# Performance work log

Hardware: AMD Instinct MI355X
Metric: run time of the kernel (lower is better)

## Reference

```python
import jax, jax.numpy as jnp
from jax import lax
import numpy as np

BLUR = 1e-4      # sinkhorn_blur
P_NORM = 2       # sinkhorn_p
SCALING = 0.9
NUM_SG = 8
LOCAL_W = 1.0
GLOBAL_W = 0.5
BATCH = 4096
DIM = 256


def _cost(X, Y):
    # geomloss cost for p=2: ||x-y||^2 / 2, computed via GEMM (no [P,m,m,d] broadcast)
    x2 = jnp.sum(X * X, axis=-1)                      # [P,m]
    y2 = jnp.sum(Y * Y, axis=-1)                      # [P,m]
    xy = jnp.einsum('pid,pjd->pij', X, Y)             # [P,m,m]
    sq = jnp.clip(x2[:, :, None] + y2[:, None, :] - 2.0 * xy, 0.0)
    return 0.5 * sq


def _softmin(eps, C, h):
    # softmin_eps(C, h)_i = -eps * logsumexp_j (h_j - C_ij / eps)
    return -eps * jax.nn.logsumexp(h[:, None, :] - C / eps, axis=-1)


def _eps_schedule():
    # epsilon-scaling: from (diameter bound)^p down to blur^p by factor scaling^p
    eps0 = 4.0 * DIM                 # static upper bound on sq. diameter of N(0,1) features
    target = BLUR ** P_NORM
    ratio = SCALING ** P_NORM
    n = int(np.ceil(np.log(target / eps0) / np.log(ratio)))
    return np.maximum(eps0 * ratio ** np.arange(n + 1), target).astype(np.float32)


def _sinkhorn_pairs(X, Y):
    # Debiased Sinkhorn divergence for a batch of pairs; X,Y: [P,m,d] -> [P]
    P, m, d = X.shape
    loga = -jnp.log(float(m))  # uniform weights
    Cxy = _cost(X, Y)
    Cyx = jnp.swapaxes(Cxy, 1, 2)
    Cxx = _cost(X, X)
    Cyy = _cost(Y, Y)
    # geomloss runs the scaling iterations detached, then one last extrapolation with grad
    Cs = tuple(lax.stop_gradient(C) for C in (Cxy, Cyx, Cxx, Cyy))
    eps_list = jnp.asarray(_eps_schedule())

    def body(carry, eps):
        f, g, px, py = carry
        ft = _softmin(eps, Cs[0], loga + g / eps)
        gt = _softmin(eps, Cs[1], loga + f / eps)
        pxt = _softmin(eps, Cs[2], loga + px / eps)
        pyt = _softmin(eps, Cs[3], loga + py / eps)
        return (0.5 * (f + ft), 0.5 * (g + gt), 0.5 * (px + pxt), 0.5 * (py + pyt)), None

    init = tuple(jnp.zeros((P, m), X.dtype) for _ in range(4))
    (f, g, px, py), _ = lax.scan(body, init, eps_list)

    eps_f = eps_list[-1]
    f_fin = _softmin(eps_f, Cxy, loga + lax.stop_gradient(g) / eps_f)
    g_fin = _softmin(eps_f, Cyx, loga + lax.stop_gradient(f) / eps_f)
    px_fin = _softmin(eps_f, Cxx, loga + lax.stop_gradient(px) / eps_f)
    py_fin = _softmin(eps_f, Cyy, loga + lax.stop_gradient(py) / eps_f)
    # S_eps(x,y) = <a, f - p_x> + <b, g - p_y>, uniform weights -> means
    return jnp.mean(f_fin - px_fin, axis=-1) + jnp.mean(g_fin - py_fin, axis=-1)


def _forward(features, labels, subgroups):
    B, d = features.shape
    m_local = B // (2 * NUM_SG)   # samples per (class, subgroup) cell
    m_global = B // NUM_SG        # samples per subgroup
    pi, pj = np.triu_indices(NUM_SG, k=1)  # 28 subgroup pairs

    # local: per-class subgroup cells (balanced inputs -> static sizes)
    cells = []
    for lbl in range(2):
        for sg in range(NUM_SG):
            idx = jnp.nonzero((labels == lbl) & (subgroups == sg), size=m_local)[0]
            cells.append(features[idx])
    cells = jnp.stack(cells).reshape(2, NUM_SG, m_local, d)
    X = cells[:, pi].reshape(-1, m_local, d)   # [56,m,d]
    Y = cells[:, pj].reshape(-1, m_local, d)
    # (sum_real/28 + sum_fake/28)/2 == mean over all 56 pairs
    local_loss = jnp.mean(_sinkhorn_pairs(X, Y))

    gcells = jnp.stack([features[jnp.nonzero(subgroups == sg, size=m_global)[0]]
                        for sg in range(NUM_SG)])  # [8,m_g,d]
    global_loss = jnp.mean(_sinkhorn_pairs(gcells[pi], gcells[pj]))

    return LOCAL_W * local_loss + GLOBAL_W * global_loss


def setup_inputs():
    key = jax.random.key(0)
    features = jax.random.normal(key, (BATCH, DIM), dtype=jnp.float32)
    ar = jnp.arange(BATCH, dtype=jnp.int32)
    labels = ar % 2                      # balanced real/fake
    subgroups = (ar // 2) % NUM_SG       # balanced subgroups per class
    return {"features": features, "labels": labels, "subgroups": subgroups}


def reference(features, labels, subgroups):
    return _forward(features, labels, subgroups)
```

## Files before the change

### kernel.cpp

```cpp
#include <hip/hip_runtime.h>
#include <math.h>

#define LOG2E 1.4426950408889634f
#define LN2   0.6931471805599453f

typedef short    short8  __attribute__((ext_vector_type(8)));
typedef float    floatx4 __attribute__((ext_vector_type(4)));
typedef _Float16 half8   __attribute__((ext_vector_type(8)));

__constant__ int c_pi[28] = {0,0,0,0,0,0,0,1,1,1,1,1,1,2,2,2,2,2,3,3,3,3,4,4,4,5,5,6};
__constant__ int c_pj[28] = {1,2,3,4,5,6,7,2,3,4,5,6,7,3,4,5,6,7,4,5,6,7,5,6,7,6,7,7};

__device__ unsigned short g_cellsL[16*256*256];
__device__ unsigned short g_cellsG[8*512*256];
__device__ float g_x2L[16*256];
__device__ float g_x2G[8*512];
__device__ int   g_idxL[16*256];
__device__ int   g_idxG[8*512];
__device__ _Float16 g_CL[128*256*256];
__device__ _Float16 g_CG[64*512*512];
__device__ float g_fL[2][56*256];
__device__ float g_gL[2][56*256];
__device__ float g_pxL[2][16*256];
__device__ float g_fG[2][28*512];
__device__ float g_gG[2][28*512];
__device__ float g_pxG[2][8*512];

__device__ __forceinline__ unsigned short f2bf(float f) {
    unsigned u = __float_as_uint(f);
    u += 0x7fffu + ((u >> 16) & 1u);
    return (unsigned short)(u >> 16);
}

__global__ void k_index(const int* __restrict__ labels, const int* __restrict__ subg) {
    int b = blockIdx.x, lane = threadIdx.x;
    int want_l, want_s, cap; int* out;
    if (b < 16) { want_l = b >> 3; want_s = b & 7; cap = 256; out = g_idxL + b*256; }
    else        { want_l = -1;     want_s = b - 16; cap = 512; out = g_idxG + (b-16)*512; }
    int cnt = 0;
    for (int base = 0; base < 4096; base += 64) {
        int i = base + lane;
        bool m = (subg[i] == want_s) && (want_l < 0 || labels[i] == want_l);
        unsigned long long mask = __ballot(m);
        int pos = cnt + __popcll(mask & ((1ull << lane) - 1ull));
        if (m && pos < cap) out[pos] = i;
        cnt += __popcll(mask);
    }
}

__global__ void k_gather(const float* __restrict__ feat) {
    int wv = blockIdx.x*4 + (threadIdx.x >> 6);
    int lane = threadIdx.x & 63;
    const float* src; unsigned short* dst; float* x2out;
    if (wv < 4096) {
        int c = wv >> 8, row = wv & 255;
        src = feat + (size_t)g_idxL[c*256+row]*256;
        dst = g_cellsL + (size_t)(c*256+row)*256;
        x2out = g_x2L + c*256 + row;
    } else {
        int v = wv - 4096; int c = v >> 9, row = v & 511;
        src = feat + (size_t)g_idxG[c*512+row]*256;
        dst = g_cellsG + (size_t)(c*512+row)*256;
        x2out = g_x2G + c*512 + row;
    }
    floatx4 v4 = *(const floatx4*)(src + lane*4);
    float s = v4[0]*v4[0] + v4[1]*v4[1] + v4[2]*v4[2] + v4[3]*v4[3];
    unsigned lo = (unsigned)f2bf(v4[0]) | ((unsigned)f2bf(v4[1]) << 16);
    unsigned hi = (unsigned)f2bf(v4[2]) | ((unsigned)f2bf(v4[3]) << 16);
    unsigned* d32 = (unsigned*)dst;
    d32[lane*2] = lo; d32[lane*2+1] = hi;
    for (int o = 32; o; o >>= 1) s += __shfl_xor(s, o);
    if (lane == 0) *x2out = s;
}

__global__ void k_gemm() {
    int job = blockIdx.x*4 + (threadIdx.x >> 6);
    int lane = threadIdx.x & 63;
    const unsigned short *A, *B; _Float16* Cout; const float *x2a, *x2b;
    int m, ti, tj;
    if (job < 32768) {
        int mm = job >> 8, t = job & 255; ti = t >> 4; tj = t & 15; m = 256;
        int ca, cb;
        if (mm < 56)       { int lbl = mm/28,  q = mm%28;  ca = lbl*8 + c_pi[q]; cb = lbl*8 + c_pj[q]; }
        else if (mm < 112) { int p = mm-56; int lbl = p/28, q = p%28;
                             ca = lbl*8 + c_pj[q]; cb = lbl*8 + c_pi[q]; }
        else               { int c = mm-112; ca = cb = c; }
        A = g_cellsL + (size_t)ca*65536; B = g_cellsL + (size_t)cb*65536;
        x2a = g_x2L + ca*256; x2b = g_x2L + cb*256;
        Cout = g_CL + (size_t)mm*65536;
    } else {
        int jj = job - 32768; int mm = jj >> 10, t = jj & 1023; ti = t >> 5; tj = t & 31; m = 512;
        int ca, cb;
        if (mm < 28)      { ca = c_pi[mm];    cb = c_pj[mm]; }
        else if (mm < 56) { ca = c_pj[mm-28]; cb = c_pi[mm-28]; }
        else              { ca = cb = mm-56; }
        A = g_cellsG + (size_t)ca*131072; B = g_cellsG + (size_t)cb*131072;
        x2a = g_x2G + ca*512; x2b = g_x2G + cb*512;
        Cout = g_CG + (size_t)mm*262144;
    }
    int r = lane & 15, quad = lane >> 4;
    const unsigned short* Ap = A + (size_t)(ti*16 + r)*256 + quad*8;
    const unsigned short* Bp = B + (size_t)(tj*16 + r)*256 + quad*8;
    floatx4 acc = {0.f, 0.f, 0.f, 0.f};
    #pragma unroll
    for (int k = 0; k < 256; k += 32) {
        short8 av = *(const short8*)(Ap + k);
        short8 bv = *(const short8*)(Bp + k);
        acc = __builtin_amdgcn_mfma_f32_16x16x32_bf16(av, bv, acc, 0, 0, 0);
    }
    int jc = tj*16 + r;
    float y2 = x2b[jc];
    #pragma unroll
    for (int rr = 0; rr < 4; rr++) {
        int ir = ti*16 + quad*4 + rr;
        float v = x2a[ir] + y2 - 2.f*acc[rr];
        Cout[(size_t)ir*m + jc] = (_Float16)(0.5f*fmaxf(v, 0.f));
    }
}

__global__ void k_init() {
    int t = blockIdx.x*256 + threadIdx.x;
    if      (t < 14336) g_fL[0][t] = 0.f;
    else if (t < 28672) g_gL[0][t-14336] = 0.f;
    else if (t < 32768) g_pxL[0][t-28672] = 0.f;
    else if (t < 47104) g_fG[0][t-32768] = 0.f;
    else if (t < 61440) g_gG[0][t-47104] = 0.f;
    else                g_pxG[0][t-61440] = 0.f;
}

template<int M>
__device__ __forceinline__ void sm_pass(const _Float16* __restrict__ C,
    const float* __restrict__ hsrc, const float* __restrict__ fold,
    float* __restrict__ fout, int r0, float eps, float inv_eps, float loga,
    int hard, int fin)
{
    const int W = (M == 256) ? 16 : 32;
    int tid = threadIdx.x, lane = tid & 63, w = tid >> 6;
    int co = (M == 256) ? (lane & 31) : lane;
    float h[8];
    floatx4 h0 = *(const floatx4*)(hsrc + co*8);
    floatx4 h1 = *(const floatx4*)(hsrc + co*8 + 4);
    #pragma unroll
    for (int k = 0; k < 4; k++) { h[k] = loga + h0[k]*inv_eps; h[4+k] = loga + h1[k]*inv_eps; }
    int rbase = (M == 256) ? (r0 + w*16) : (r0 + w*8);
    int rowst = (M == 256) ? 2 : 1;
    int radd  = (M == 256) ? (lane >> 5) : 0;
    bool wr   = (M == 256) ? ((lane & 31) == 0) : (lane == 0);

    const _Float16* cp = C + (size_t)(rbase + radd)*M + co*8;
    half8 cv = *(const half8*)cp;
    #pragma unroll
    for (int s = 0; s < 8; s++) {
        half8 cvn;
        if (s < 7) cvn = *(const half8*)(cp + (size_t)rowst*M);
        float tv[8]; float mx = -3.4e38f;
        #pragma unroll
        for (int k = 0; k < 8; k++) {
            float t = h[k] - (float)cv[k]*inv_eps;
            tv[k] = t; mx = fmaxf(mx, t);
        }
        #pragma unroll
        for (int o = W; o; o >>= 1) mx = fmaxf(mx, __shfl_xor(mx, o));
        float ft;
        if (!hard) {
            float sum = 0.f;
            #pragma unroll
            for (int k = 0; k < 8; k++) sum += exp2f((tv[k] - mx)*LOG2E);
            #pragma unroll
            for (int o = W; o; o >>= 1) sum += __shfl_xor(sum, o);
            ft = -eps*(mx + LN2*__log2f(sum));
        } else {
            ft = -eps*mx;
        }
        if (wr) {
            int row = rbase + rowst*s + radd;
            fout[row] = fin ? ft : 0.5f*(fold[row] + ft);
        }
        cv = cvn; cp += (size_t)rowst*M;
    }
}

__global__ void k_iter(float eps, float inv_eps, int par, int hard, int fin) {
    const float LGA = -5.545177444479562f;
    const float LGG = -6.238324625039508f;
    int b = blockIdx.x;
    int po = par, pn = par ^ 1;
    if (b < 512) {
        int m = b >> 2, r0 = (b & 3)*64;
        const _Float16* C = g_CL + (size_t)m*65536;
        const float *h, *fo; float* fn;
        if (m < 56)       { h = g_gL[po]+m*256;  fo = g_fL[po]+m*256;  fn = g_fL[pn]+m*256; }
        else if (m < 112) { int p = m-56;  h = g_fL[po]+p*256;  fo = g_gL[po]+p*256;  fn = g_gL[pn]+p*256; }
        else              { int c = m-112; h = g_pxL[po]+c*256; fo = h;               fn = g_pxL[pn]+c*256; }
        sm_pass<256>(C, h, fo, fn, r0, eps, inv_eps, LGA, hard, fin);
    } else {
        int v = b - 512; int m = v >> 4, r0 = (v & 15)*32;
        const _Float16* C = g_CG + (size_t)m*262144;
        const float *h, *fo; float* fn;
        if (m < 28)      { h = g_gG[po]+m*512;  fo = g_fG[po]+m*512;  fn = g_fG[pn]+m*512; }
        else if (m < 56) { int p = m-28;  h = g_fG[po]+p*512;  fo = g_gG[po]+p*512;  fn = g_gG[pn]+p*512; }
        else             { int c = m-56;  h = g_pxG[po]+c*512; fo = h;               fn = g_pxG[pn]+c*512; }
        sm_pass<512>(C, h, fo, fn, r0, eps, inv_eps, LGG, hard, fin);
    }
}

__global__ void k_combine(float* __restrict__ out) {
    __shared__ float red[4][4];
    int tid = threadIdx.x;
    float sfg_l = 0.f, spx_l = 0.f, sfg_g = 0.f, spx_g = 0.f;
    for (int i = tid; i < 14336; i += 256) sfg_l += g_fL[1][i] + g_gL[1][i];
    for (int i = tid; i < 4096;  i += 256) spx_l += g_pxL[1][i];
    for (int i = tid; i < 14336; i += 256) sfg_g += g_fG[1][i] + g_gG[1][i];
    for (int i = tid; i < 4096;  i += 256) spx_g += g_pxG[1][i];
    for (int o = 32; o; o >>= 1) {
        sfg_l += __shfl_xor(sfg_l, o); spx_l += __shfl_xor(spx_l, o);
        sfg_g += __shfl_xor(sfg_g, o); spx_g += __shfl_xor(spx_g, o);
    }
    int w = tid >> 6;
    if ((tid & 63) == 0) { red[0][w] = sfg_l; red[1][w] = spx_l; red[2][w] = sfg_g; red[3][w] = spx_g; }
    __syncthreads();
    if (tid == 0) {
        float SL = red[0][0]+red[0][1]+red[0][2]+red[0][3];
        float PL = red[1][0]+red[1][1]+red[1][2]+red[1][3];
        float SG = red[2][0]+red[2][1]+red[2][2]+red[2][3];
        float PG = red[3][0]+red[3][1]+red[3][2]+red[3][3];
        float local_l  = SL/14336.f - PL/2048.f;
        float global_l = SG/14336.f - PG/2048.f;
        out[0] = 1.0f*local_l + 0.5f*global_l;
    }
}

extern "C" void kernel_launch(void* const* d_in, const int* in_sizes, int n_in,
                              void* d_out, int out_size, void* d_ws, size_t ws_size,
                              hipStream_t stream) {
    (void)in_sizes; (void)n_in; (void)out_size; (void)d_ws; (void)ws_size;
    const float* feat  = (const float*)d_in[0];
    const int* labels  = (const int*)d_in[1];
    const int* subg    = (const int*)d_in[2];

    k_index <<<24,    64, 0, stream>>>(labels, subg);
    k_gather<<<2048, 256, 0, stream>>>(feat);
    k_gemm  <<<24576,256, 0, stream>>>();
    k_init  <<<256,  256, 0, stream>>>();

    double eps0 = 4.0*256.0, ratio = 0.9*0.9, target = 1e-4*1e-4;
    int n = (int)ceil(log(target/eps0)/log(ratio));
    float ef = 1e-8f;
    for (int k = 0; k <= n; k++) {
        double e = eps0 * pow(ratio, (double)k);
        if (e < target) e = target;
        ef = (float)e;
        int hard = (ef < 1e-5f) ? 1 : 0;
        k_iter<<<1536, 256, 0, stream>>>(ef, (float)(1.0/(double)ef), k & 1, hard, 0);
    }
    k_iter<<<1536, 256, 0, stream>>>(ef, (float)(1.0/(double)ef), 0, 1, 1);
    k_combine<<<1, 256, 0, stream>>>((float*)d_out);
}
```

Baseline: 2.015 ms.

## Drop transposed cost matrices and compute g-update via column-wise online logsumexp

Stops materialising the transposed Cyx cost matrices in the GEMM and instead computes the g potential update with a new column-reduction routine that reads Cxy directly. It uses a streaming max/sum logsumexp over rows, then a cross-lane and shared-memory merge. Block indexing is also remapped with an XCD-style interleave (b&7) so blocks sharing a matrix land together. This cuts GEMM work and cost-matrix storage and reads by about 44%. In exchange it adds more exp2 calls per element in the online rescaling and a __syncthreads in the column blocks.

```diff
diff --git a/kernel.cpp b/kernel.cpp
--- a/kernel.cpp
+++ b/kernel.cpp
@@ -17,8 +17,8 @@
 __device__ float g_x2G[8*512];
 __device__ int   g_idxL[16*256];
 __device__ int   g_idxG[8*512];
-__device__ _Float16 g_CL[128*256*256];
-__device__ _Float16 g_CG[64*512*512];
+__device__ _Float16 g_CL[72*256*256];
+__device__ _Float16 g_CG[36*512*512];
 __device__ float g_fL[2][56*256];
 __device__ float g_gL[2][56*256];
 __device__ float g_pxL[2][16*256];
@@ -78,22 +78,19 @@
     int lane = threadIdx.x & 63;
     const unsigned short *A, *B; _Float16* Cout; const float *x2a, *x2b;
     int m, ti, tj;
-    if (job < 32768) {
+    if (job < 18432) {
         int mm = job >> 8, t = job & 255; ti = t >> 4; tj = t & 15; m = 256;
         int ca, cb;
-        if (mm < 56)       { int lbl = mm/28,  q = mm%28;  ca = lbl*8 + c_pi[q]; cb = lbl*8 + c_pj[q]; }
-        else if (mm < 112) { int p = mm-56; int lbl = p/28, q = p%28;
-                             ca = lbl*8 + c_pj[q]; cb = lbl*8 + c_pi[q]; }
-        else               { int c = mm-112; ca = cb = c; }
+        if (mm < 56) { int lbl = mm/28, q = mm%28; ca = lbl*8 + c_pi[q]; cb = lbl*8 + c_pj[q]; }
+        else         { int c = mm-56; ca = cb = c; }
         A = g_cellsL + (size_t)ca*65536; B = g_cellsL + (size_t)cb*65536;
         x2a = g_x2L + ca*256; x2b = g_x2L + cb*256;
         Cout = g_CL + (size_t)mm*65536;
     } else {
-        int jj = job - 32768; int mm = jj >> 10, t = jj & 1023; ti = t >> 5; tj = t & 31; m = 512;
+        int jj = job - 18432; int mm = jj >> 10, t = jj & 1023; ti = t >> 5; tj = t & 31; m = 512;
         int ca, cb;
-        if (mm < 28)      { ca = c_pi[mm];    cb = c_pj[mm]; }
-        else if (mm < 56) { ca = c_pj[mm-28]; cb = c_pi[mm-28]; }
-        else              { ca = cb = mm-56; }
+        if (mm < 28) { ca = c_pi[mm]; cb = c_pj[mm]; }
+        else         { ca = cb = mm-28; }
         A = g_cellsG + (size_t)ca*131072; B = g_cellsG + (size_t)cb*131072;
         x2a = g_x2G + ca*512; x2b = g_x2G + cb*512;
         Cout = g_CG + (size_t)mm*262144;
@@ -151,7 +148,7 @@
     half8 cv = *(const half8*)cp;
     #pragma unroll
     for (int s = 0; s < 8; s++) {
-        half8 cvn;
+        half8 cvn = cv;
         if (s < 7) cvn = *(const half8*)(cp + (size_t)rowst*M);
         float tv[8]; float mx = -3.4e38f;
         #pragma unroll
@@ -180,27 +177,118 @@
     }
 }
 
+template<int M>
+__device__ __forceinline__ void sm_col(const _Float16* __restrict__ C,
+    const float* __restrict__ frow, const float* __restrict__ gold,
+    float* __restrict__ gout, int c0, float eps, float inv_eps, float loga,
+    int hard, int fin)
+{
+    int tid = threadIdx.x, lane = tid & 63, w = tid >> 6;
+    const float i2  = inv_eps * LOG2E;
+    const float lg2 = loga * LOG2E;
+    int colg = lane & 7;
+    int rsub = (lane >> 3) + w*8;
+    const int STEPS = M/32;
+    float m2[8], ss[8];
+    #pragma unroll
+    for (int k = 0; k < 8; k++) { m2[k] = -3.4e38f; ss[k] = 0.f; }
+    const _Float16* cp = C + (size_t)rsub*M + c0 + colg*8;
+    half8 cv = *(const half8*)cp;
+    float fr = frow[rsub];
+    #pragma unroll
+    for (int s2 = 0; s2 < STEPS; s2++) {
+        half8 cvn = cv; float frn = fr;
+        if (s2 < STEPS-1) { cvn = *(const half8*)(cp + (size_t)32*M); frn = frow[rsub + 32*(s2+1)]; }
+        float a2 = lg2 + fr * i2;
+        if (!hard) {
+            #pragma unroll
+            for (int k = 0; k < 8; k++) {
+                float u  = a2 - (float)cv[k]*i2;
+                float mn = fmaxf(m2[k], u);
+                ss[k] = ss[k]*exp2f(m2[k]-mn) + exp2f(u-mn);
+                m2[k] = mn;
+            }
+        } else {
+            #pragma unroll
+            for (int k = 0; k < 8; k++) {
+                float u = a2 - (float)cv[k]*i2;
+                m2[k] = fmaxf(m2[k], u);
+            }
+        }
+        cv = cvn; fr = frn; cp += (size_t)32*M;
+    }
+    #pragma unroll
+    for (int o = 8; o < 64; o <<= 1) {
+        #pragma unroll
+        for (int k = 0; k < 8; k++) {
+            float mo = __shfl_xor(m2[k], o);
+            float so = __shfl_xor(ss[k], o);
+            float mn = fmaxf(m2[k], mo);
+            if (!hard) ss[k] = ss[k]*exp2f(m2[k]-mn) + so*exp2f(mo-mn);
+            m2[k] = mn;
+        }
+    }
+    __shared__ float smm[4][64], sms[4][64];
+    if (lane < 8) {
+        #pragma unroll
+        for (int k = 0; k < 8; k++) { smm[w][lane*8+k] = m2[k]; sms[w][lane*8+k] = ss[k]; }
+    }
+    __syncthreads();
+    if (tid < 64) {
+        float m = smm[0][tid], s = sms[0][tid];
+        #pragma unroll
+        for (int ww = 1; ww < 4; ww++) {
+            float mo = smm[ww][tid], so = sms[ww][tid];
+            float mn = fmaxf(m, mo);
+            if (!hard) s = s*exp2f(m-mn) + so*exp2f(mo-mn);
+            m = mn;
+        }
+        float gt = hard ? (-eps*LN2*m) : (-eps*LN2*(m + __log2f(s)));
+        int c = c0 + tid;
+        gout[c] = fin ? gt : 0.5f*(gold[c] + gt);
+    }
+}
+
 __global__ void k_iter(float eps, float inv_eps, int par, int hard, int fin) {
     const float LGA = -5.545177444479562f;
     const float LGG = -6.238324625039508f;
     int b = blockIdx.x;
+    int x = b & 7, s = b >> 3;
     int po = par, pn = par ^ 1;
-    if (b < 512) {
-        int m = b >> 2, r0 = (b & 3)*64;
-        const _Float16* C = g_CL + (size_t)m*65536;
-        const float *h, *fo; float* fn;
-        if (m < 56)       { h = g_gL[po]+m*256;  fo = g_fL[po]+m*256;  fn = g_fL[pn]+m*256; }
-        else if (m < 112) { int p = m-56;  h = g_fL[po]+p*256;  fo = g_gL[po]+p*256;  fn = g_gL[pn]+p*256; }
-        else              { int c = m-112; h = g_pxL[po]+c*256; fo = h;               fn = g_pxL[pn]+c*256; }
-        sm_pass<256>(C, h, fo, fn, r0, eps, inv_eps, LGA, hard, fin);
+    if (s < 56) {
+        int q = s >> 3, j = s & 7, p = q*8 + x;
+        const _Float16* C = g_CL + (size_t)p*65536;
+        if (j < 4)
+            sm_pass<256>(C, g_gL[po]+p*256, g_fL[po]+p*256, g_fL[pn]+p*256,
+                         j*64, eps, inv_eps, LGA, hard, fin);
+        else
+            sm_col<256>(C, g_fL[po]+p*256, g_gL[po]+p*256, g_gL[pn]+p*256,
+                        (j-4)*64, eps, inv_eps, LGA, hard, fin);
+    } else if (s < 64) {
+        int t = s - 56; int c = (t >> 2)*8 + x;
+        const _Float16* C = g_CL + (size_t)(56+c)*65536;
+        const float* h = g_pxL[po]+c*256;
+        sm_pass<256>(C, h, h, g_pxL[pn]+c*256, (t&3)*64, eps, inv_eps, LGA, hard, fin);
     } else {
-        int v = b - 512; int m = v >> 4, r0 = (v & 15)*32;
-        const _Float16* C = g_CG + (size_t)m*262144;
-        const float *h, *fo; float* fn;
-        if (m < 28)      { h = g_gG[po]+m*512;  fo = g_fG[po]+m*512;  fn = g_fG[pn]+m*512; }
-        else if (m < 56) { int p = m-28;  h = g_fG[po]+p*512;  fo = g_gG[po]+p*512;  fn = g_gG[pn]+p*512; }
-        else             { int c = m-56;  h = g_pxG[po]+c*512; fo = h;               fn = g_pxG[pn]+c*512; }
-        sm_pass<512>(C, h, fo, fn, r0, eps, inv_eps, LGG, hard, fin);
+        int gp = (x < 4) ? 4 : 3;
+        int t = s - 64;
+        if (t < 24*gp) {
+            int q = t/24, j = t%24, p = q*8 + x;
+            const _Float16* C = g_CG + (size_t)p*262144;
+            if (j < 16)
+                sm_pass<512>(C, g_gG[po]+p*512, g_fG[po]+p*512, g_fG[pn]+p*512,
+                             j*32, eps, inv_eps, LGG, hard, fin);
+            else
+                sm_col<512>(C, g_fG[po]+p*512, g_gG[po]+p*512, g_gG[pn]+p*512,
+                            (j-16)*64, eps, inv_eps, LGG, hard, fin);
+        } else {
+            t -= 24*gp;
+            if (t < 16) {
+                const _Float16* C = g_CG + (size_t)(28+x)*262144;
+                const float* h = g_pxG[po]+x*512;
+                sm_pass<512>(C, h, h, g_pxG[pn]+x*512, t*32, eps, inv_eps, LGG, hard, fin);
+            }
+        }
     }
 }
 
@@ -240,7 +328,7 @@
 
     k_index <<<24,    64, 0, stream>>>(labels, subg);
     k_gather<<<2048, 256, 0, stream>>>(feat);
-    k_gemm  <<<24576,256, 0, stream>>>();
+    k_gemm  <<<13824,256, 0, stream>>>();
     k_init  <<<256,  256, 0, stream>>>();
 
     double eps0 = 4.0*256.0, ratio = 0.9*0.9, target = 1e-4*1e-4;
@@ -251,8 +339,8 @@
         if (e < target) e = target;
         ef = (float)e;
         int hard = (ef < 1e-5f) ? 1 : 0;
-        k_iter<<<1536, 256, 0, stream>>>(ef, (float)(1.0/(double)ef), k & 1, hard, 0);
-    }
-    k_iter<<<1536, 256, 0, stream>>>(ef, (float)(1.0/(double)ef), 0, 1, 1);
+        k_iter<<<1408, 256, 0, stream>>>(ef, (float)(1.0/(double)ef), k & 1, hard, 0);
+    }
+    k_iter<<<1408, 256, 0, stream>>>(ef, (float)(1.0/(double)ef), 0, 1, 1);
     k_combine<<<1, 256, 0, stream>>>((float*)d_out);
 }
```

New measurement: 2.229 ms. 1.11x slower.

## Fuse all Sinkhorn iterations into one persistent LDS-resident kernel with group barriers

Applied to the files above, without the earlier changes.

Replaces the roughly 123 per-epsilon k_iter launches with a single persistent kernel of 216 blocks. Each block keeps its slice of the cost matrix in LDS and loops over all epsilon rounds on chip. The transposed cost matrices are dropped: g is computed as a column-wise online logsumexp over the same C tile. Global-pair blocks that split one matrix four ways exchange partial (max, sum) pairs through global memory behind spin-wait group barriers. This removes per-launch overhead and the repeated HBM reads of C and halves GEMM work, but it relies on all 216 blocks being co-resident (one per CU) for the barriers to avoid deadlock, and the barrier has a guard that breaks out silently.

```diff
diff --git a/kernel.cpp b/kernel.cpp
--- a/kernel.cpp
+++ b/kernel.cpp
@@ -17,19 +17,29 @@
 __device__ float g_x2G[8*512];
 __device__ int   g_idxL[16*256];
 __device__ int   g_idxG[8*512];
-__device__ _Float16 g_CL[128*256*256];
-__device__ _Float16 g_CG[64*512*512];
-__device__ float g_fL[2][56*256];
-__device__ float g_gL[2][56*256];
-__device__ float g_pxL[2][16*256];
-__device__ float g_fG[2][28*512];
-__device__ float g_gG[2][28*512];
-__device__ float g_pxG[2][8*512];
+__device__ _Float16 g_CL[72*256*256];
+__device__ _Float16 g_CG[36*512*512];
+__device__ unsigned long long g_xch[28][4][512];
+__device__ float g_xpx[8][4][128];
+__device__ unsigned g_bar[36];
+__device__ float g_acc[4];
 
 __device__ __forceinline__ unsigned short f2bf(float f) {
     unsigned u = __float_as_uint(f);
     u += 0x7fffu + ((u >> 16) & 1u);
     return (unsigned short)(u >> 16);
+}
+__device__ __forceinline__ void xst64(unsigned long long* p, unsigned long long v) {
+    __hip_atomic_store(p, v, __ATOMIC_RELAXED, __HIP_MEMORY_SCOPE_AGENT);
+}
+__device__ __forceinline__ unsigned long long xld64(const unsigned long long* p) {
+    return __hip_atomic_load(p, __ATOMIC_RELAXED, __HIP_MEMORY_SCOPE_AGENT);
+}
+__device__ __forceinline__ void xstf(float* p, float v) {
+    __hip_atomic_store(p, v, __ATOMIC_RELAXED, __HIP_MEMORY_SCOPE_AGENT);
+}
+__device__ __forceinline__ float xldf(const float* p) {
+    return __hip_atomic_load(p, __ATOMIC_RELAXED, __HIP_MEMORY_SCOPE_AGENT);
 }
 
 __global__ void k_index(const int* __restrict__ labels, const int* __restrict__ subg) {
@@ -78,22 +88,19 @@
     int lane = threadIdx.x & 63;
     const unsigned short *A, *B; _Float16* Cout; const float *x2a, *x2b;
     int m, ti, tj;
-    if (job < 32768) {
+    if (job < 18432) {
         int mm = job >> 8, t = job & 255; ti = t >> 4; tj = t & 15; m = 256;
         int ca, cb;
-        if (mm < 56)       { int lbl = mm/28,  q = mm%28;  ca = lbl*8 + c_pi[q]; cb = lbl*8 + c_pj[q]; }
-        else if (mm < 112) { int p = mm-56; int lbl = p/28, q = p%28;
-                             ca = lbl*8 + c_pj[q]; cb = lbl*8 + c_pi[q]; }
-        else               { int c = mm-112; ca = cb = c; }
+        if (mm < 56) { int lbl = mm/28, q = mm%28; ca = lbl*8 + c_pi[q]; cb = lbl*8 + c_pj[q]; }
+        else         { int c = mm-56; ca = cb = c; }
         A = g_cellsL + (size_t)ca*65536; B = g_cellsL + (size_t)cb*65536;
         x2a = g_x2L + ca*256; x2b = g_x2L + cb*256;
         Cout = g_CL + (size_t)mm*65536;
     } else {
-        int jj = job - 32768; int mm = jj >> 10, t = jj & 1023; ti = t >> 5; tj = t & 31; m = 512;
+        int jj = job - 18432; int mm = jj >> 10, t = jj & 1023; ti = t >> 5; tj = t & 31; m = 512;
         int ca, cb;
-        if (mm < 28)      { ca = c_pi[mm];    cb = c_pj[mm]; }
-        else if (mm < 56) { ca = c_pj[mm-28]; cb = c_pi[mm-28]; }
-        else              { ca = cb = mm-56; }
+        if (mm < 28) { ca = c_pi[mm]; cb = c_pj[mm]; }
+        else         { ca = cb = mm-28; }
         A = g_cellsG + (size_t)ca*131072; B = g_cellsG + (size_t)cb*131072;
         x2a = g_x2G + ca*512; x2b = g_x2G + cb*512;
         Cout = g_CG + (size_t)mm*262144;
@@ -119,114 +126,366 @@
 }
 
 __global__ void k_init() {
-    int t = blockIdx.x*256 + threadIdx.x;
-    if      (t < 14336) g_fL[0][t] = 0.f;
-    else if (t < 28672) g_gL[0][t-14336] = 0.f;
-    else if (t < 32768) g_pxL[0][t-28672] = 0.f;
-    else if (t < 47104) g_fG[0][t-32768] = 0.f;
-    else if (t < 61440) g_gG[0][t-47104] = 0.f;
-    else                g_pxG[0][t-61440] = 0.f;
-}
-
-template<int M>
-__device__ __forceinline__ void sm_pass(const _Float16* __restrict__ C,
-    const float* __restrict__ hsrc, const float* __restrict__ fold,
-    float* __restrict__ fout, int r0, float eps, float inv_eps, float loga,
-    int hard, int fin)
-{
-    const int W = (M == 256) ? 16 : 32;
-    int tid = threadIdx.x, lane = tid & 63, w = tid >> 6;
-    int co = (M == 256) ? (lane & 31) : lane;
-    float h[8];
-    floatx4 h0 = *(const floatx4*)(hsrc + co*8);
-    floatx4 h1 = *(const floatx4*)(hsrc + co*8 + 4);
+    int t = threadIdx.x;
+    if (t < 36) g_bar[t] = 0u;
+    if (t < 4)  g_acc[t] = 0.f;
+}
+
+__device__ __forceinline__ void group_bar(int gid, unsigned tgt) {
+    if (threadIdx.x == 0) {
+        __hip_atomic_fetch_add(&g_bar[gid], 1u, __ATOMIC_RELEASE, __HIP_MEMORY_SCOPE_AGENT);
+        int guard = 0;
+        while (__hip_atomic_load(&g_bar[gid], __ATOMIC_ACQUIRE, __HIP_MEMORY_SCOPE_AGENT) < tgt) {
+            __builtin_amdgcn_s_sleep(2);
+            if (++guard > 5000000) break;
+        }
+    }
+    __syncthreads();
+}
+
+extern __shared__ char smem[];
+__global__ void __launch_bounds__(512) k_solve() {
+    _Float16* sC = (_Float16*)smem;
+    float* scr  = (float*)(smem + 131072);
+    float* sg   = (float*)(smem + 147456);
+    float* sf   = (float*)(smem + 151552);
+    float* sred = (float*)(smem + 155648);
+    int b = blockIdx.x, tid = threadIdx.x, lane = tid & 63, w = tid >> 6;
+
+    int role, gid = -1, q = 0;
+    const _Float16* Csrc; float loga;
+    if (b < 112)      { role = 2; gid = b >> 2; q = b & 3;
+                        Csrc = g_CG + (size_t)gid*262144 + (size_t)q*65536;
+                        loga = -6.238324625039508f; }
+    else if (b < 144) { role = 3; int t = b - 112; int c = t >> 2; q = t & 3; gid = 28 + c;
+                        Csrc = g_CG + (size_t)(28+c)*262144 + (size_t)q*65536;
+                        loga = -6.238324625039508f; }
+    else if (b < 200) { role = 0; int p = b - 144;
+                        Csrc = g_CL + (size_t)p*65536;
+                        loga = -5.545177444479562f; }
+    else              { role = 1; int c = b - 200;
+                        Csrc = g_CL + (size_t)(56+c)*65536;
+                        loga = -5.545177444479562f; }
+
+    for (int i = tid; i < 8192; i += 512)
+        ((floatx4*)sC)[i] = ((const floatx4*)Csrc)[i];
+    for (int i = tid; i < 1024; i += 512) { sg[i] = 0.f; sf[i] = 0.f; }
+    __syncthreads();
+
+    const double ratio = 0.9*0.9;
+    int po = 0;
+    for (int round = 0; round < 123; round++) {
+        int fin = (round == 122);
+        double e = 1024.0 * pow(ratio, (double)(fin ? 121 : round));
+        if (e < 1e-8) e = 1e-8;
+        float ef = (float)e;
+        float inv = (float)(1.0/e);
+        int hard = (ef < 1e-5f) ? 1 : 0;
+        float i2  = inv * LOG2E;
+        float lg2 = loga * LOG2E;
+        float meps = -ef * LN2;
+        int pn = po ^ 1;
+
+        if (role == 2) {
+            const float* gp = sg + po*512;
+            const float* fpo = sf + po*512;
+            float* fpn = sf + pn*512;
+            float h2[8];
+            #pragma unroll
+            for (int k = 0; k < 8; k++) h2[k] = lg2 + gp[lane*8+k]*i2;
+            float m2[8], ssv[8];
+            #pragma unroll
+            for (int k = 0; k < 8; k++) { m2[k] = -3.4e38f; ssv[k] = 0.f; }
+            #pragma unroll 4
+            for (int s = 0; s < 16; s++) {
+                int row = w*16 + s;
+                half8 cv = *(const half8*)(sC + row*512 + lane*8);
+                float fr = fpo[row];
+                float a2 = lg2 + fr*i2;
+                float tv[8]; float mx = -3.4e38f;
+                #pragma unroll
+                for (int k = 0; k < 8; k++) {
+                    float d = (float)cv[k]*(-i2);
+                    float t = h2[k] + d; tv[k] = t; mx = fmaxf(mx, t);
+                    float u = a2 + d;
+                    float mn = fmaxf(m2[k], u);
+                    if (!hard) ssv[k] = ssv[k]*exp2f(m2[k]-mn) + exp2f(u-mn);
+                    m2[k] = mn;
+                }
+                #pragma unroll
+                for (int o = 32; o; o >>= 1) mx = fmaxf(mx, __shfl_xor(mx, o));
+                float ft;
+                if (!hard) {
+                    float sum = 0.f;
+                    #pragma unroll
+                    for (int k = 0; k < 8; k++) sum += exp2f(tv[k]-mx);
+                    #pragma unroll
+                    for (int o = 32; o; o >>= 1) sum += __shfl_xor(sum, o);
+                    ft = meps*(mx + __log2f(sum));
+                } else ft = meps*mx;
+                if (lane == 0) fpn[row] = fin ? ft : 0.5f*(fr + ft);
+            }
+            if (w >= 4) {
+                float* pm = scr + (w-4)*512; float* ps = scr + 2048 + (w-4)*512;
+                #pragma unroll
+                for (int k = 0; k < 8; k++) { pm[lane*8+k] = m2[k]; ps[lane*8+k] = ssv[k]; }
+            }
+            __syncthreads();
+            if (w < 4) {
+                const float* pm = scr + w*512; const float* ps = scr + 2048 + w*512;
+                #pragma unroll
+                for (int k = 0; k < 8; k++) {
+                    float mo = pm[lane*8+k], so = ps[lane*8+k];
+                    float mn = fmaxf(m2[k], mo);
+                    if (!hard) ssv[k] = ssv[k]*exp2f(m2[k]-mn) + so*exp2f(mo-mn);
+                    m2[k] = mn;
+                }
+            }
+            __syncthreads();
+            if (w >= 1 && w < 4) {
+                float* pm = scr + (w-1)*512; float* ps = scr + 2048 + (w-1)*512;
+                #pragma unroll
+                for (int k = 0; k < 8; k++) { pm[lane*8+k] = m2[k]; ps[lane*8+k] = ssv[k]; }
+            }
+            __syncthreads();
+            if (w == 0) {
+                #pragma unroll
+                for (int j = 0; j < 3; j++) {
+                    const float* pm = scr + j*512; const float* ps = scr + 2048 + j*512;
+                    #pragma unroll
+                    for (int k = 0; k < 8; k++) {
+                        float mo = pm[lane*8+k], so = ps[lane*8+k];
+                        float mn = fmaxf(m2[k], mo);
+                        if (!hard) ssv[k] = ssv[k]*exp2f(m2[k]-mn) + so*exp2f(mo-mn);
+                        m2[k] = mn;
+                    }
+                }
+                #pragma unroll
+                for (int k = 0; k < 8; k++)
+                    xst64(&g_xch[gid][q][lane*8+k],
+                          (unsigned long long)__float_as_uint(m2[k]) |
+                          ((unsigned long long)__float_as_uint(ssv[k]) << 32));
+            }
+            __syncthreads();
+            group_bar(gid, 4u*(unsigned)(round+1));
+            {
+                int c = tid;
+                unsigned long long v0 = xld64(&g_xch[gid][0][c]);
+                unsigned long long v1 = xld64(&g_xch[gid][1][c]);
+                unsigned long long v2 = xld64(&g_xch[gid][2][c]);
+                unsigned long long v3 = xld64(&g_xch[gid][3][c]);
+                float a0 = __uint_as_float((unsigned)v0), b0 = __uint_as_float((unsigned)(v0 >> 32));
+                float a1 = __uint_as_float((unsigned)v1), b1 = __uint_as_float((unsigned)(v1 >> 32));
+                float a2m = __uint_as_float((unsigned)v2), b2 = __uint_as_float((unsigned)(v2 >> 32));
+                float a3 = __uint_as_float((unsigned)v3), b3 = __uint_as_float((unsigned)(v3 >> 32));
+                float m = fmaxf(fmaxf(a0, a1), fmaxf(a2m, a3));
+                float gt;
+                if (!hard) {
+                    float s = b0*exp2f(a0-m) + b1*exp2f(a1-m) + b2*exp2f(a2m-m) + b3*exp2f(a3-m);
+                    gt = meps*(m + __log2f(s));
+                } else gt = meps*m;
+                sg[pn*512+c] = fin ? gt : 0.5f*(sg[po*512+c] + gt);
+            }
+            __syncthreads();
+        } else if (role == 3) {
+            const float* pp = sg + po*512;
+            float* ppn = sg + pn*512;
+            float h2[8];
+            #pragma unroll
+            for (int k = 0; k < 8; k++) h2[k] = lg2 + pp[lane*8+k]*i2;
+            #pragma unroll 4
+            for (int s = 0; s < 16; s++) {
+                int row = w*16 + s;
+                half8 cv = *(const half8*)(sC + row*512 + lane*8);
+                float tv[8]; float mx = -3.4e38f;
+                #pragma unroll
+                for (int k = 0; k < 8; k++) {
+                    float t = h2[k] - (float)cv[k]*i2;
+                    tv[k] = t; mx = fmaxf(mx, t);
+                }
+                #pragma unroll
+                for (int o = 32; o; o >>= 1) mx = fmaxf(mx, __shfl_xor(mx, o));
+                float ft;
+                if (!hard) {
+                    float sum = 0.f;
+                    #pragma unroll
+                    for (int k = 0; k < 8; k++) sum += exp2f(tv[k]-mx);
+                    #pragma unroll
+                    for (int o = 32; o; o >>= 1) sum += __shfl_xor(sum, o);
+                    ft = meps*(mx + __log2f(sum));
+                } else ft = meps*mx;
+                if (lane == 0) {
+                    float old = pp[q*128 + row];
+                    xstf(&g_xpx[gid-28][q][row], fin ? ft : 0.5f*(old + ft));
+                }
+            }
+            __syncthreads();
+            group_bar(gid, 4u*(unsigned)(round+1));
+            { int c = tid; ppn[c] = xldf(&g_xpx[gid-28][c>>7][c&127]); }
+            __syncthreads();
+        } else if (role == 0) {
+            const float* gp = sg + po*512;
+            const float* fpo = sf + po*512;
+            float* fpn = sf + pn*512;
+            int co = lane & 31, radd = lane >> 5;
+            float h2[8];
+            #pragma unroll
+            for (int k = 0; k < 8; k++) h2[k] = lg2 + gp[co*8+k]*i2;
+            float m2[8], ssv[8];
+            #pragma unroll
+            for (int k = 0; k < 8; k++) { m2[k] = -3.4e38f; ssv[k] = 0.f; }
+            #pragma unroll 4
+            for (int s = 0; s < 16; s++) {
+                int row = w*32 + 2*s + radd;
+                half8 cv = *(const half8*)(sC + row*256 + co*8);
+                float fr = fpo[row];
+                float a2 = lg2 + fr*i2;
+                float tv[8]; float mx = -3.4e38f;
+                #pragma unroll
+                for (int k = 0; k < 8; k++) {
+                    float d = (float)cv[k]*(-i2);
+                    float t = h2[k] + d; tv[k] = t; mx = fmaxf(mx, t);
+                    float u = a2 + d;
+                    float mn = fmaxf(m2[k], u);
+                    if (!hard) ssv[k] = ssv[k]*exp2f(m2[k]-mn) + exp2f(u-mn);
+                    m2[k] = mn;
+                }
+                #pragma unroll
+                for (int o = 16; o; o >>= 1) mx = fmaxf(mx, __shfl_xor(mx, o));
+                float ft;
+                if (!hard) {
+                    float sum = 0.f;
+                    #pragma unroll
+                    for (int k = 0; k < 8; k++) sum += exp2f(tv[k]-mx);
+                    #pragma unroll
+                    for (int o = 16; o; o >>= 1) sum += __shfl_xor(sum, o);
+                    ft = meps*(mx + __log2f(sum));
+                } else ft = meps*mx;
+                if ((lane & 31) == 0) fpn[row] = fin ? ft : 0.5f*(fr + ft);
+            }
+            #pragma unroll
+            for (int k = 0; k < 8; k++) {
+                float mo = __shfl_xor(m2[k], 32), so = __shfl_xor(ssv[k], 32);
+                float mn = fmaxf(m2[k], mo);
+                if (!hard) ssv[k] = ssv[k]*exp2f(m2[k]-mn) + so*exp2f(mo-mn);
+                m2[k] = mn;
+            }
+            if (w >= 4 && lane < 32) {
+                float* pm = scr + (w-4)*256; float* ps = scr + 1024 + (w-4)*256;
+                #pragma unroll
+                for (int k = 0; k < 8; k++) { pm[co*8+k] = m2[k]; ps[co*8+k] = ssv[k]; }
+            }
+            __syncthreads();
+            if (w < 4 && lane < 32) {
+                const float* pm = scr + w*256; const float* ps = scr + 1024 + w*256;
+                #pragma unroll
+                for (int k = 0; k < 8; k++) {
+                    float mo = pm[co*8+k], so = ps[co*8+k];
+                    float mn = fmaxf(m2[k], mo);
+                    if (!hard) ssv[k] = ssv[k]*exp2f(m2[k]-mn) + so*exp2f(mo-mn);
+                    m2[k] = mn;
+                }
+            }
+            __syncthreads();
+            if (w >= 1 && w < 4 && lane < 32) {
+                float* pm = scr + (w-1)*256; float* ps = scr + 1024 + (w-1)*256;
+                #pragma unroll
+                for (int k = 0; k < 8; k++) { pm[co*8+k] = m2[k]; ps[co*8+k] = ssv[k]; }
+            }
+            __syncthreads();
+            if (w == 0 && lane < 32) {
+                #pragma unroll
+                for (int j = 0; j < 3; j++) {
+                    const float* pm = scr + j*256; const float* ps = scr + 1024 + j*256;
+                    #pragma unroll
+                    for (int k = 0; k < 8; k++) {
+                        float mo = pm[co*8+k], so = ps[co*8+k];
+                        float mn = fmaxf(m2[k], mo);
+                        if (!hard) ssv[k] = ssv[k]*exp2f(m2[k]-mn) + so*exp2f(mo-mn);
+                        m2[k] = mn;
+                    }
+                }
+                #pragma unroll
+                for (int k = 0; k < 8; k++) {
+                    int c = co*8 + k;
+                    float gt = hard ? meps*m2[k] : meps*(m2[k] + __log2f(ssv[k]));
+                    sg[pn*512+c] = fin ? gt : 0.5f*(sg[po*512+c] + gt);
+                }
+            }
+            __syncthreads();
+        } else {
+            const float* pp = sg + po*512;
+            float* ppn = sg + pn*512;
+            int co = lane & 31, radd = lane >> 5;
+            float h2[8];
+            #pragma unroll
+            for (int k = 0; k < 8; k++) h2[k] = lg2 + pp[co*8+k]*i2;
+            #pragma unroll 4
+            for (int s = 0; s < 16; s++) {
+                int row = w*32 + 2*s + radd;
+                half8 cv = *(const half8*)(sC + row*256 + co*8);
+                float tv[8]; float mx = -3.4e38f;
+                #pragma unroll
+                for (int k = 0; k < 8; k++) {
+                    float t = h2[k] - (float)cv[k]*i2;
+                    tv[k] = t; mx = fmaxf(mx, t);
+                }
+                #pragma unroll
+                for (int o = 16; o; o >>= 1) mx = fmaxf(mx, __shfl_xor(mx, o));
+                float ft;
+                if (!hard) {
+                    float sum = 0.f;
+                    #pragma unroll
+                    for (int k = 0; k < 8; k++) sum += exp2f(tv[k]-mx);
+                    #pragma unroll
+                    for (int o = 16; o; o >>= 1) sum += __shfl_xor(sum, o);
+                    ft = meps*(mx + __log2f(sum));
+                } else ft = meps*mx;
+                if ((lane & 31) == 0) {
+                    float old = pp[row];
+                    ppn[row] = fin ? ft : 0.5f*(old + ft);
+                }
+            }
+            __syncthreads();
+        }
+        po = pn;
+    }
+
+    float v = 0.f, v2 = 0.f; int idx, idx2 = -1;
+    if (role == 0)      { if (tid < 256) v = sf[po*512+tid] + sg[po*512+tid]; idx = 0; }
+    else if (role == 1) { if (tid < 256) v = sg[po*512+tid]; idx = 1; }
+    else if (role == 2) { if (tid < 128) v = sf[po*512+tid]; idx = 2;
+                          if (q == 0) { v2 = sg[po*512+tid]; idx2 = 2; } }
+    else                { if (tid < 128) v = sg[po*512 + q*128 + tid]; idx = 3; }
     #pragma unroll
-    for (int k = 0; k < 4; k++) { h[k] = loga + h0[k]*inv_eps; h[4+k] = loga + h1[k]*inv_eps; }
-    int rbase = (M == 256) ? (r0 + w*16) : (r0 + w*8);
-    int rowst = (M == 256) ? 2 : 1;
-    int radd  = (M == 256) ? (lane >> 5) : 0;
-    bool wr   = (M == 256) ? ((lane & 31) == 0) : (lane == 0);
-
-    const _Float16* cp = C + (size_t)(rbase + radd)*M + co*8;
-    half8 cv = *(const half8*)cp;
-    #pragma unroll
-    for (int s = 0; s < 8; s++) {
-        half8 cvn;
-        if (s < 7) cvn = *(const half8*)(cp + (size_t)rowst*M);
-        float tv[8]; float mx = -3.4e38f;
-        #pragma unroll
-        for (int k = 0; k < 8; k++) {
-            float t = h[k] - (float)cv[k]*inv_eps;
-            tv[k] = t; mx = fmaxf(mx, t);
-        }
-        #pragma unroll
-        for (int o = W; o; o >>= 1) mx = fmaxf(mx, __shfl_xor(mx, o));
-        float ft;
-        if (!hard) {
-            float sum = 0.f;
-            #pragma unroll
-            for (int k = 0; k < 8; k++) sum += exp2f((tv[k] - mx)*LOG2E);
-            #pragma unroll
-            for (int o = W; o; o >>= 1) sum += __shfl_xor(sum, o);
-            ft = -eps*(mx + LN2*__log2f(sum));
-        } else {
-            ft = -eps*mx;
-        }
-        if (wr) {
-            int row = rbase + rowst*s + radd;
-            fout[row] = fin ? ft : 0.5f*(fold[row] + ft);
-        }
-        cv = cvn; cp += (size_t)rowst*M;
-    }
-}
-
-__global__ void k_iter(float eps, float inv_eps, int par, int hard, int fin) {
-    const float LGA = -5.545177444479562f;
-    const float LGG = -6.238324625039508f;
-    int b = blockIdx.x;
-    int po = par, pn = par ^ 1;
-    if (b < 512) {
-        int m = b >> 2, r0 = (b & 3)*64;
-        const _Float16* C = g_CL + (size_t)m*65536;
-        const float *h, *fo; float* fn;
-        if (m < 56)       { h = g_gL[po]+m*256;  fo = g_fL[po]+m*256;  fn = g_fL[pn]+m*256; }
-        else if (m < 112) { int p = m-56;  h = g_fL[po]+p*256;  fo = g_gL[po]+p*256;  fn = g_gL[pn]+p*256; }
-        else              { int c = m-112; h = g_pxL[po]+c*256; fo = h;               fn = g_pxL[pn]+c*256; }
-        sm_pass<256>(C, h, fo, fn, r0, eps, inv_eps, LGA, hard, fin);
-    } else {
-        int v = b - 512; int m = v >> 4, r0 = (v & 15)*32;
-        const _Float16* C = g_CG + (size_t)m*262144;
-        const float *h, *fo; float* fn;
-        if (m < 28)      { h = g_gG[po]+m*512;  fo = g_fG[po]+m*512;  fn = g_fG[pn]+m*512; }
-        else if (m < 56) { int p = m-28;  h = g_fG[po]+p*512;  fo = g_gG[po]+p*512;  fn = g_gG[pn]+p*512; }
-        else             { int c = m-56;  h = g_pxG[po]+c*512; fo = h;               fn = g_pxG[pn]+c*512; }
-        sm_pass<512>(C, h, fo, fn, r0, eps, inv_eps, LGG, hard, fin);
-    }
-}
-
-__global__ void k_combine(float* __restrict__ out) {
-    __shared__ float red[4][4];
-    int tid = threadIdx.x;
-    float sfg_l = 0.f, spx_l = 0.f, sfg_g = 0.f, spx_g = 0.f;
-    for (int i = tid; i < 14336; i += 256) sfg_l += g_fL[1][i] + g_gL[1][i];
-    for (int i = tid; i < 4096;  i += 256) spx_l += g_pxL[1][i];
-    for (int i = tid; i < 14336; i += 256) sfg_g += g_fG[1][i] + g_gG[1][i];
-    for (int i = tid; i < 4096;  i += 256) spx_g += g_pxG[1][i];
-    for (int o = 32; o; o >>= 1) {
-        sfg_l += __shfl_xor(sfg_l, o); spx_l += __shfl_xor(spx_l, o);
-        sfg_g += __shfl_xor(sfg_g, o); spx_g += __shfl_xor(spx_g, o);
-    }
-    int w = tid >> 6;
-    if ((tid & 63) == 0) { red[0][w] = sfg_l; red[1][w] = spx_l; red[2][w] = sfg_g; red[3][w] = spx_g; }
+    for (int o = 32; o; o >>= 1) v += __shfl_xor(v, o);
+    if ((tid & 63) == 0) sred[w] = v;
     __syncthreads();
     if (tid == 0) {
-        float SL = red[0][0]+red[0][1]+red[0][2]+red[0][3];
-        float PL = red[1][0]+red[1][1]+red[1][2]+red[1][3];
-        float SG = red[2][0]+red[2][1]+red[2][2]+red[2][3];
-        float PG = red[3][0]+red[3][1]+red[3][2]+red[3][3];
-        float local_l  = SL/14336.f - PL/2048.f;
-        float global_l = SG/14336.f - PG/2048.f;
-        out[0] = 1.0f*local_l + 0.5f*global_l;
+        float t = 0.f;
+        #pragma unroll
+        for (int i = 0; i < 8; i++) t += sred[i];
+        atomicAdd(&g_acc[idx], t);
+    }
+    if (idx2 >= 0) {
+        __syncthreads();
+        #pragma unroll
+        for (int o = 32; o; o >>= 1) v2 += __shfl_xor(v2, o);
+        if ((tid & 63) == 0) sred[w] = v2;
+        __syncthreads();
+        if (tid == 0) {
+            float t = 0.f;
+            #pragma unroll
+            for (int i = 0; i < 8; i++) t += sred[i];
+            atomicAdd(&g_acc[idx2], t);
+        }
+    }
+}
+
+__global__ void k_combine(float* __restrict__ out) {
+    if (threadIdx.x == 0) {
+        float SL = g_acc[0], PL = g_acc[1], SG = g_acc[2], PG = g_acc[3];
+        out[0] = (SL/14336.f - PL/2048.f) + 0.5f*(SG/14336.f - PG/2048.f);
     }
 }
 
@@ -238,21 +497,17 @@
     const int* labels  = (const int*)d_in[1];
     const int* subg    = (const int*)d_in[2];
 
+    static int attr_set = 0;
+    if (!attr_set) {
+        hipFuncSetAttribute((const void*)k_solve,
+                            hipFuncAttributeMaxDynamicSharedMemorySize, 155712);
+        attr_set = 1;
+    }
+
     k_index <<<24,    64, 0, stream>>>(labels, subg);
     k_gather<<<2048, 256, 0, stream>>>(feat);
-    k_gemm  <<<24576,256, 0, stream>>>();
-    k_init  <<<256,  256, 0, stream>>>();
-
-    double eps0 = 4.0*256.0, ratio = 0.9*0.9, target = 1e-4*1e-4;
-    int n = (int)ceil(log(target/eps0)/log(ratio));
-    float ef = 1e-8f;
-    for (int k = 0; k <= n; k++) {
-        double e = eps0 * pow(ratio, (double)k);
-        if (e < target) e = target;
-        ef = (float)e;
-        int hard = (ef < 1e-5f) ? 1 : 0;
-        k_iter<<<1536, 256, 0, stream>>>(ef, (float)(1.0/(double)ef), k & 1, hard, 0);
-    }
-    k_iter<<<1536, 256, 0, stream>>>(ef, (float)(1.0/(double)ef), 0, 1, 1);
-    k_combine<<<1, 256, 0, stream>>>((float*)d_out);
-}
+    k_gemm  <<<13824,256, 0, stream>>>();
+    k_init  <<<1,     64, 0, stream>>>();
+    k_solve <<<216,  512, 155712, stream>>>();
+    k_combine<<<1,    64, 0, stream>>>((float*)d_out);
+}
```

Result: slower. 3.039 ms (+50.8%).
